# Optimization experiments

Hardware: AMD Instinct MI355X
Metric: run time of the kernel (lower is better)

Reference implementation:

```python
import jax, jax.numpy as jnp
import numpy as np

T, N, D, G, H = 52, 1000, 2, 150, 50


def _mlp_scalar(x, W1, b1, W2, b2):
    # Elementwise scalar-input MLP: x [T,N,D] -> [T,N,D]
    h = jnp.tanh(x[..., None] * W1[0] + b1)          # [T,N,D,H]
    return jnp.einsum('tndh,h->tnd', h, W2[:, 0]) + b2[0]


def setup_inputs() -> dict:
    key = jax.random.key(0)
    ks = jax.random.split(key, 18)
    f = lambda k, s: jax.random.normal(k, s, dtype=jnp.float32)
    return {
        'TX': f(ks[0], (T, N, D)),
        't': jnp.arange(T, dtype=jnp.float32) * 0.01,
        'gaussn_0': f(ks[1], (G, T - 2, N)),
        'gaussn_1': f(ks[2], (G, T - 2, N, D)),
        'gaussn_2': f(ks[3], (G, T - 2, N, D)),
        'gaussnp1_1': f(ks[4], (G, T - 2, N, D)),
        'gaussnp1_2': f(ks[5], (G, T - 2, N, D)),
        'gaussnp2_0': f(ks[6], (G, T - 2, N)),
        'gaussnp2_1': f(ks[7], (G, T - 2, N, D)),
        'gaussnp2_2': f(ks[8], (G, T - 2, N, D)),
        'Wd1': f(ks[9], (1, H)) * 0.5,
        'bd1': jnp.zeros((H,), jnp.float32),
        'Wd2': f(ks[10], (H, 1)) * (1.0 / np.sqrt(H)),
        'bd2': jnp.zeros((1,), jnp.float32),
        'Ws1': f(ks[11], (1, H)) * 0.5,
        'bs1': jnp.zeros((H,), jnp.float32),
        'Ws2': f(ks[12], (H, 1)) * (1.0 / np.sqrt(H)),
        'bs2': jnp.zeros((1,), jnp.float32),
    }


def reference(TX, t, gaussn_0, gaussn_1, gaussn_2, gaussnp1_1, gaussnp1_2,
              gaussnp2_0, gaussnp2_1, gaussnp2_2,
              Wd1, bd1, Wd2, bd2, Ws1, bs1, Ws2, bs2):
    n = TX.shape[1]
    drift = _mlp_scalar(TX, Wd1, bd1, Wd2, bd2)            # [T,N,D]
    Dh = 0.5 * _mlp_scalar(TX, Ws1, bs1, Ws2, bs2)          # [T,N,D]

    def proj(g1, g2, a):
        # sum over d then mean over n == einsum over (n,d) / n -> [G, T-2]
        return (jnp.einsum('gtnd,tnd->gt', g1, a[0])
                + jnp.einsum('gtnd,tnd->gt', g2, a[1])) / n

    An = proj(gaussn_1, gaussn_2, (drift[:-2], Dh[:-2]))
    Anp1 = proj(gaussnp1_1, gaussnp1_2, (drift[1:-1], Dh[1:-1]))
    Anp2 = proj(gaussnp2_1, gaussnp2_2, (drift[2:], Dh[2:]))

    dt = (jnp.max(t) - jnp.min(t)) / (TX.shape[0] - 1)
    Aq = (An + 4.0 * Anp1 + Anp2) / 3.0 * dt                # LMM_3
    bq = jnp.mean(gaussnp2_0, axis=2) - jnp.mean(gaussn_0, axis=2)
    return (Aq - bq).reshape(-1)                            # [G*(T-2)]
```

## Files before the change

kernel.cpp:

```cpp
#include <hip/hip_runtime.h>
#include <hip/hip_bf16.h>

#define T_   52
#define N_   1000
#define D_   2
#define G_   150
#define H_   50
#define TM2  (T_ - 2)
#define ND   (N_ * D_)
#define TND  (T_ * N_ * D_)

typedef unsigned short ushort8_t __attribute__((ext_vector_type(8)));
typedef float          float8_t  __attribute__((ext_vector_type(8)));

__device__ __forceinline__ float bf2f(unsigned short u) {
    return __uint_as_float(((unsigned)u) << 16);
}
__device__ __forceinline__ unsigned short f2bf(float f) {
    unsigned u = __float_as_uint(f);
    u += 0x7fffu + ((u >> 16) & 1u);
    return (unsigned short)(u >> 16);
}

template<bool F32>
__device__ __forceinline__ float ld1(const void* p, int i) {
    if constexpr (F32) return ((const float*)p)[i];
    else               return bf2f(((const unsigned short*)p)[i]);
}

template<bool F32>
__device__ __forceinline__ float8_t ld8(const void* p, int i) {
    if constexpr (F32) {
        return *(const float8_t*)((const float*)p + i);
    } else {
        ushort8_t v = *(const ushort8_t*)((const unsigned short*)p + i);
        float8_t r;
#pragma unroll
        for (int j = 0; j < 8; ++j) r[j] = bf2f(v[j]);
        return r;
    }
}

template<bool F32>
__device__ __forceinline__ void mlp_body(
    const void* __restrict__ TX,
    const void* __restrict__ Wd1, const void* __restrict__ bd1,
    const void* __restrict__ Wd2, const void* __restrict__ bd2,
    const void* __restrict__ Ws1, const void* __restrict__ bs1,
    const void* __restrict__ Ws2, const void* __restrict__ bs2,
    float* __restrict__ drift, float* __restrict__ Dh)
{
    __shared__ float sW[6][H_];
    const int tid = threadIdx.x;
    if (tid < H_) {
        sW[0][tid] = ld1<F32>(Wd1, tid);
        sW[1][tid] = ld1<F32>(bd1, tid);
        sW[2][tid] = ld1<F32>(Wd2, tid);
        sW[3][tid] = ld1<F32>(Ws1, tid);
        sW[4][tid] = ld1<F32>(bs1, tid);
        sW[5][tid] = ld1<F32>(Ws2, tid);
    }
    __syncthreads();
    const int i = blockIdx.x * 256 + tid;
    if (i >= TND) return;
    const float x = ld1<F32>(TX, i);
    float accd = 0.f, accs = 0.f;
#pragma unroll 10
    for (int h = 0; h < H_; ++h) {
        accd += tanhf(fmaf(x, sW[0][h], sW[1][h])) * sW[2][h];
        accs += tanhf(fmaf(x, sW[3][h], sW[4][h])) * sW[5][h];
    }
    drift[i] = accd + ld1<F32>(bd2, 0);
    Dh[i]    = 0.5f * (accs + ld1<F32>(bs2, 0));
}

__global__ __launch_bounds__(256) void mlp_kernel(
    const void* TX,
    const void* Wd1, const void* bd1, const void* Wd2, const void* bd2,
    const void* Ws1, const void* bs1, const void* Ws2, const void* bs2,
    const void* t, float* drift, float* Dh)
{
    if (((const unsigned*)t)[0] == 0u)
        mlp_body<true>(TX, Wd1, bd1, Wd2, bd2, Ws1, bs1, Ws2, bs2, drift, Dh);
    else
        mlp_body<false>(TX, Wd1, bd1, Wd2, bd2, Ws1, bs1, Ws2, bs2, drift, Dh);
}

template<bool F32>
__device__ __forceinline__ void proj_body(
    const void* __restrict__ gn0,  const void* __restrict__ gn1,
    const void* __restrict__ gn2,  const void* __restrict__ gp11,
    const void* __restrict__ gp12, const void* __restrict__ gp20,
    const void* __restrict__ gp21, const void* __restrict__ gp22,
    const float* __restrict__ drift, const float* __restrict__ Dh,
    const void* __restrict__ t, void* __restrict__ out)
{
    const int gid = blockIdx.x;
    const int tp  = gid % TM2;
    const int tid = threadIdx.x;

    float acc = 0.f, bacc = 0.f;

    if (tid < ND / 8) {
        const int base = gid * ND + tid * 8;
        const float8_t a1 = ld8<F32>(gn1,  base);
        const float8_t a2 = ld8<F32>(gn2,  base);
        const float8_t b1 = ld8<F32>(gp11, base);
        const float8_t b2 = ld8<F32>(gp12, base);
        const float8_t c1 = ld8<F32>(gp21, base);
        const float8_t c2 = ld8<F32>(gp22, base);
        const int cb = tp * ND + tid * 8;
        const float8_t d0 = *(const float8_t*)(drift + cb);
        const float8_t h0 = *(const float8_t*)(Dh    + cb);
        const float8_t d1 = *(const float8_t*)(drift + cb + ND);
        const float8_t h1 = *(const float8_t*)(Dh    + cb + ND);
        const float8_t d2 = *(const float8_t*)(drift + cb + 2 * ND);
        const float8_t h2 = *(const float8_t*)(Dh    + cb + 2 * ND);
#pragma unroll
        for (int j = 0; j < 8; ++j) {
            acc += a1[j] * d0[j] + a2[j] * h0[j]
                 + 4.f * (b1[j] * d1[j] + b2[j] * h1[j])
                 + c1[j] * d2[j] + c2[j] * h2[j];
        }
    }
    if (tid < N_ / 8) {
        const int b0 = gid * N_ + tid * 8;
        const float8_t z0 = ld8<F32>(gn0,  b0);
        const float8_t z2 = ld8<F32>(gp20, b0);
#pragma unroll
        for (int j = 0; j < 8; ++j) bacc += z2[j] - z0[j];
    }

#pragma unroll
    for (int off = 32; off > 0; off >>= 1) {
        acc  += __shfl_down(acc, off);
        bacc += __shfl_down(bacc, off);
    }
    __shared__ float sA[4], sB[4];
    const int wave = tid >> 6, lane = tid & 63;
    if (lane == 0) { sA[wave] = acc; sB[wave] = bacc; }
    __syncthreads();
    if (tid == 0) {
        const float A = sA[0] + sA[1] + sA[2] + sA[3];
        const float B = sB[0] + sB[1] + sB[2] + sB[3];
        const float dt = (ld1<F32>(t, T_ - 1) - ld1<F32>(t, 0)) * (1.0f / (T_ - 1));
        const float val = A * (dt / (3.0f * (float)N_)) - B * (1.0f / (float)N_);
        if constexpr (F32) ((float*)out)[gid] = val;
        else               ((unsigned short*)out)[gid] = f2bf(val);
    }
}

__global__ __launch_bounds__(256) void proj_kernel(
    const void* gn0,  const void* gn1,  const void* gn2,
    const void* gp11, const void* gp12, const void* gp20,
    const void* gp21, const void* gp22,
    const float* drift, const float* Dh,
    const void* t, void* out)
{
    if (((const unsigned*)t)[0] == 0u)
        proj_body<true>(gn0, gn1, gn2, gp11, gp12, gp20, gp21, gp22,
                        drift, Dh, t, out);
    else
        proj_body<false>(gn0, gn1, gn2, gp11, gp12, gp20, gp21, gp22,
                         drift, Dh, t, out);
}

extern "C" void kernel_launch(void* const* d_in, const int* in_sizes, int n_in,
                              void* d_out, int out_size, void* d_ws, size_t ws_size,
                              hipStream_t stream) {
    const void* TX   = d_in[0];
    const void* t    = d_in[1];
    const void* gn0  = d_in[2];
    const void* gn1  = d_in[3];
    const void* gn2  = d_in[4];
    const void* gp11 = d_in[5];
    const void* gp12 = d_in[6];
    const void* gp20 = d_in[7];
    const void* gp21 = d_in[8];
    const void* gp22 = d_in[9];
    const void* Wd1  = d_in[10];
    const void* bd1  = d_in[11];
    const void* Wd2  = d_in[12];
    const void* bd2  = d_in[13];
    const void* Ws1  = d_in[14];
    const void* bs1  = d_in[15];
    const void* Ws2  = d_in[16];
    const void* bs2  = d_in[17];

    float* drift = (float*)d_ws;
    float* Dh    = drift + TND;

    mlp_kernel<<<(TND + 255) / 256, 256, 0, stream>>>(
        TX, Wd1, bd1, Wd2, bd2, Ws1, bs1, Ws2, bs2, t, drift, Dh);

    proj_kernel<<<G_ * TM2, 256, 0, stream>>>(
        gn0, gn1, gn2, gp11, gp12, gp20, gp21, gp22, drift, Dh, t,
        (void*)d_out);
}
```

Measured before the change: 401.5 us.

## Replace per-row projection blocks with grid-stride streaming and segmented atomics

The projection kernel used to launch one 256-thread block per (g,t) row. Only 250 threads loaded data and the rest idled. It now runs a fixed grid of 2048 blocks that stream all elements contiguously with full waves. Each wave reduces its partial sums, and because a wave can span a row boundary, the sums are split into at most two row segments and added to a workspace with atomics. A zero kernel and a finalize kernel are added, which means two extra launches, atomic contention, and float summation order that is no longer deterministic.

```diff
diff --git a/kernel.cpp b/kernel.cpp
--- a/kernel.cpp
+++ b/kernel.cpp
@@ -9,6 +9,12 @@
 #define TM2  (T_ - 2)
 #define ND   (N_ * D_)
 #define TND  (T_ * N_ * D_)
+#define NWG  (G_ * TM2)
+#define LA   (G_ * TM2 * ND)
+#define LB   (G_ * TM2 * N_)
+#define CA   (LA / 8)
+#define CB   (LB / 8)
+#define STREAM_BLOCKS 2048
 
 typedef unsigned short ushort8_t __attribute__((ext_vector_type(8)));
 typedef float          float8_t  __attribute__((ext_vector_type(8)));
@@ -39,6 +45,11 @@
         for (int j = 0; j < 8; ++j) r[j] = bf2f(v[j]);
         return r;
     }
+}
+
+__global__ __launch_bounds__(256) void zero_kernel(float* __restrict__ ws) {
+    const int i = blockIdx.x * 256 + threadIdx.x;
+    if (i < 2 * NWG) ws[i] = 0.f;
 }
 
 template<bool F32>
@@ -86,83 +97,117 @@
         mlp_body<false>(TX, Wd1, bd1, Wd2, bd2, Ws1, bs1, Ws2, bs2, drift, Dh);
 }
 
-template<bool F32>
-__device__ __forceinline__ void proj_body(
+__device__ __forceinline__ void seg_atomic(float s, int r, float* dst, bool valid)
+{
+    s = valid ? s : 0.f;
+    const int r0  = __shfl(r, 0);
+    const int r63 = __shfl(r, 63);
+    float lo = (r == r0) ? s : 0.f;
+    float hi = s - lo;
+#pragma unroll
+    for (int off = 32; off > 0; off >>= 1) {
+        lo += __shfl_down(lo, off);
+        hi += __shfl_down(hi, off);
+    }
+    if ((threadIdx.x & 63) == 0) {
+        atomicAdd(dst + r0, lo);
+        if (r63 != r0) atomicAdd(dst + r63, hi);
+    }
+}
+
+template<bool F32>
+__device__ __forceinline__ void stream_body(
     const void* __restrict__ gn0,  const void* __restrict__ gn1,
     const void* __restrict__ gn2,  const void* __restrict__ gp11,
     const void* __restrict__ gp12, const void* __restrict__ gp20,
     const void* __restrict__ gp21, const void* __restrict__ gp22,
     const float* __restrict__ drift, const float* __restrict__ Dh,
-    const void* __restrict__ t, void* __restrict__ out)
-{
-    const int gid = blockIdx.x;
-    const int tp  = gid % TM2;
-    const int tid = threadIdx.x;
-
-    float acc = 0.f, bacc = 0.f;
-
-    if (tid < ND / 8) {
-        const int base = gid * ND + tid * 8;
-        const float8_t a1 = ld8<F32>(gn1,  base);
-        const float8_t a2 = ld8<F32>(gn2,  base);
-        const float8_t b1 = ld8<F32>(gp11, base);
-        const float8_t b2 = ld8<F32>(gp12, base);
-        const float8_t c1 = ld8<F32>(gp21, base);
-        const float8_t c2 = ld8<F32>(gp22, base);
-        const int cb = tp * ND + tid * 8;
+    float* __restrict__ wsA, float* __restrict__ wsB)
+{
+    const int lane  = threadIdx.x & 63;
+    const int nth   = gridDim.x * 256;
+    const int wbase = blockIdx.x * 256 + (threadIdx.x & ~63);
+
+    for (int k0 = wbase; k0 < CA; k0 += nth) {
+        const int k     = k0 + lane;
+        const bool valid = (k < CA);
+        const int e  = (valid ? k : CA - 1) * 8;
+        const int r  = e / ND;
+        const int j  = e - r * ND;
+        const int tp = r % TM2;
+        const int cb = tp * ND + j;
+
+        const float8_t a1 = ld8<F32>(gn1,  e);
+        const float8_t a2 = ld8<F32>(gn2,  e);
+        const float8_t b1 = ld8<F32>(gp11, e);
+        const float8_t b2 = ld8<F32>(gp12, e);
+        const float8_t c1 = ld8<F32>(gp21, e);
+        const float8_t c2 = ld8<F32>(gp22, e);
         const float8_t d0 = *(const float8_t*)(drift + cb);
         const float8_t h0 = *(const float8_t*)(Dh    + cb);
         const float8_t d1 = *(const float8_t*)(drift + cb + ND);
         const float8_t h1 = *(const float8_t*)(Dh    + cb + ND);
         const float8_t d2 = *(const float8_t*)(drift + cb + 2 * ND);
         const float8_t h2 = *(const float8_t*)(Dh    + cb + 2 * ND);
-#pragma unroll
-        for (int j = 0; j < 8; ++j) {
-            acc += a1[j] * d0[j] + a2[j] * h0[j]
-                 + 4.f * (b1[j] * d1[j] + b2[j] * h1[j])
-                 + c1[j] * d2[j] + c2[j] * h2[j];
+
+        float s = 0.f;
+#pragma unroll
+        for (int q = 0; q < 8; ++q) {
+            s += a1[q] * d0[q] + a2[q] * h0[q]
+               + 4.f * (b1[q] * d1[q] + b2[q] * h1[q])
+               + c1[q] * d2[q] + c2[q] * h2[q];
         }
-    }
-    if (tid < N_ / 8) {
-        const int b0 = gid * N_ + tid * 8;
-        const float8_t z0 = ld8<F32>(gn0,  b0);
-        const float8_t z2 = ld8<F32>(gp20, b0);
-#pragma unroll
-        for (int j = 0; j < 8; ++j) bacc += z2[j] - z0[j];
-    }
-
-#pragma unroll
-    for (int off = 32; off > 0; off >>= 1) {
-        acc  += __shfl_down(acc, off);
-        bacc += __shfl_down(bacc, off);
-    }
-    __shared__ float sA[4], sB[4];
-    const int wave = tid >> 6, lane = tid & 63;
-    if (lane == 0) { sA[wave] = acc; sB[wave] = bacc; }
-    __syncthreads();
-    if (tid == 0) {
-        const float A = sA[0] + sA[1] + sA[2] + sA[3];
-        const float B = sB[0] + sB[1] + sB[2] + sB[3];
-        const float dt = (ld1<F32>(t, T_ - 1) - ld1<F32>(t, 0)) * (1.0f / (T_ - 1));
-        const float val = A * (dt / (3.0f * (float)N_)) - B * (1.0f / (float)N_);
-        if constexpr (F32) ((float*)out)[gid] = val;
-        else               ((unsigned short*)out)[gid] = f2bf(val);
-    }
-}
-
-__global__ __launch_bounds__(256) void proj_kernel(
+        seg_atomic(s, r, wsA, valid);
+    }
+
+    for (int k0 = wbase; k0 < CB; k0 += nth) {
+        const int k     = k0 + lane;
+        const bool valid = (k < CB);
+        const int e = (valid ? k : CB - 1) * 8;
+        const int r = e / N_;
+
+        const float8_t z0 = ld8<F32>(gn0,  e);
+        const float8_t z2 = ld8<F32>(gp20, e);
+        float s = 0.f;
+#pragma unroll
+        for (int q = 0; q < 8; ++q) s += z2[q] - z0[q];
+        seg_atomic(s, r, wsB, valid);
+    }
+}
+
+__global__ __launch_bounds__(256) void stream_kernel(
     const void* gn0,  const void* gn1,  const void* gn2,
     const void* gp11, const void* gp12, const void* gp20,
     const void* gp21, const void* gp22,
     const float* drift, const float* Dh,
-    const void* t, void* out)
+    const void* t, float* wsA, float* wsB)
 {
     if (((const unsigned*)t)[0] == 0u)
-        proj_body<true>(gn0, gn1, gn2, gp11, gp12, gp20, gp21, gp22,
-                        drift, Dh, t, out);
+        stream_body<true>(gn0, gn1, gn2, gp11, gp12, gp20, gp21, gp22,
+                          drift, Dh, wsA, wsB);
     else
-        proj_body<false>(gn0, gn1, gn2, gp11, gp12, gp20, gp21, gp22,
-                         drift, Dh, t, out);
+        stream_body<false>(gn0, gn1, gn2, gp11, gp12, gp20, gp21, gp22,
+                           drift, Dh, wsA, wsB);
+}
+
+template<bool F32>
+__device__ __forceinline__ void fin_body(
+    const float* __restrict__ wsA, const float* __restrict__ wsB,
+    const void* __restrict__ t, void* __restrict__ out)
+{
+    const int b = blockIdx.x * 256 + threadIdx.x;
+    if (b >= NWG) return;
+    const float dt  = (ld1<F32>(t, T_ - 1) - ld1<F32>(t, 0)) * (1.0f / (T_ - 1));
+    const float val = wsA[b] * (dt / (3.0f * (float)N_)) - wsB[b] * (1.0f / (float)N_);
+    if constexpr (F32) ((float*)out)[b] = val;
+    else               ((unsigned short*)out)[b] = f2bf(val);
+}
+
+__global__ __launch_bounds__(256) void fin_kernel(
+    const float* wsA, const float* wsB, const void* t, void* out)
+{
+    if (((const unsigned*)t)[0] == 0u) fin_body<true>(wsA, wsB, t, out);
+    else                               fin_body<false>(wsA, wsB, t, out);
 }
 
 extern "C" void kernel_launch(void* const* d_in, const int* in_sizes, int n_in,
@@ -187,13 +232,18 @@
     const void* Ws2  = d_in[16];
     const void* bs2  = d_in[17];
 
-    float* drift = (float*)d_ws;
+    float* wsA   = (float*)d_ws;
+    float* wsB   = wsA + NWG;
+    float* drift = wsB + NWG;
     float* Dh    = drift + TND;
+
+    zero_kernel<<<(2 * NWG + 255) / 256, 256, 0, stream>>>(wsA);
 
     mlp_kernel<<<(TND + 255) / 256, 256, 0, stream>>>(
         TX, Wd1, bd1, Wd2, bd2, Ws1, bs1, Ws2, bs2, t, drift, Dh);
 
-    proj_kernel<<<G_ * TM2, 256, 0, stream>>>(
-        gn0, gn1, gn2, gp11, gp12, gp20, gp21, gp22, drift, Dh, t,
-        (void*)d_out);
-}
+    stream_kernel<<<STREAM_BLOCKS, 256, 0, stream>>>(
+        gn0, gn1, gn2, gp11, gp12, gp20, gp21, gp22, drift, Dh, t, wsA, wsB);
+
+    fin_kernel<<<(NWG + 255) / 256, 256, 0, stream>>>(wsA, wsB, t, d_out);
+}
```

New measurement: 413.5 us. 3.0% more time.
